# Optimization experiments

Hardware: AMD Instinct MI355X
Metric: run time of the kernel (lower is better)

## Reference

```python
import jax, jax.numpy as jnp
import numpy as np

N_NODES = 100000
N_EDGES = 6400000
F_IN = 128
F_OUT = 16


def setup_inputs() -> dict:
    key = jax.random.key(0)
    k1, k2, k3 = jax.random.split(key, 3)
    x = jax.random.normal(k1, (N_NODES, F_IN), dtype=jnp.float32)
    edge_index = jax.random.randint(k2, (2, N_EDGES), 0, N_NODES, dtype=jnp.int64)
    W = jax.random.normal(k3, (F_IN, F_OUT), dtype=jnp.float32) / np.sqrt(F_IN)
    b = jnp.zeros((F_OUT,), dtype=jnp.float32)
    return {"x": x, "edge_index": edge_index, "W": W, "b": b}


def reference(x, edge_index, W, b):
    # GCNConv (PyG defaults: add self-loops, symmetric normalization) -> tanh -> mean pool
    N = x.shape[0]
    loops = jnp.arange(N, dtype=edge_index.dtype)
    row = jnp.concatenate([edge_index[0], loops])  # source nodes
    col = jnp.concatenate([edge_index[1], loops])  # target nodes
    # degree of target nodes (edge weight 1.0)
    deg = jax.ops.segment_sum(jnp.ones(row.shape[0], dtype=x.dtype), col, num_segments=N)
    dinv = jnp.where(deg > 0, jax.lax.rsqrt(deg), 0.0)
    norm = dinv[row] * dinv[col]  # [E+N]
    h = x @ W  # [N, F_OUT] transform first (cheaper than transforming messages)
    msgs = h[row] * norm[:, None]  # gather + scale
    out = jax.ops.segment_sum(msgs, col, num_segments=N) + b  # scatter-add
    h = jnp.tanh(out)
    # MeanAggregation over all nodes -> single graph embedding [1, F_OUT]
    return jnp.mean(h, axis=0, keepdims=True)
```

## Files before the change

### kernel.cpp

```cpp
#include <hip/hip_runtime.h>
#include <math.h>

#define N_NODES 100000
#define N_EDGES 6400000
#define F_IN 128
#define F_OUT 16
#define NB 391
#define NBLK 1600
#define EPB 4000
#define LOCW 392
#define KPB 8
#define QSCALE 1024.0f
#define QINV   (1.0f / 1024.0f)
#define FIN_GRID 640

__global__ void __launch_bounds__(256) count_kernel(const int* __restrict__ col,
                                                    int* __restrict__ loc,
                                                    int* __restrict__ deg,
                                                    int* __restrict__ acc) {
    __shared__ int hist[NB];
    const int t = threadIdx.x, k = blockIdx.x;
    const int z0 = k * 63;
    for (int j = t; j < 63; j += 256)
        if (z0 + j < N_NODES) deg[z0 + j] = 0;
    const int a0 = k * 1000;
    for (int j = t; j < 1000; j += 256) acc[a0 + j] = 0;
    for (int i = t; i < NB; i += 256) hist[i] = 0;
    __syncthreads();
    const int e0 = k * EPB;
    for (int i = t; i < EPB; i += 256) atomicAdd(&hist[col[e0 + i] >> 8], 1);
    __syncthreads();
    for (int b = t; b < NB; b += 256) loc[k * LOCW + b] = hist[b];
}

__global__ void __launch_bounds__(256) desta_kernel(const int* __restrict__ loc,
        int* __restrict__ destT, int* __restrict__ total) {
    __shared__ int tsum[256];
    const int t = threadIdx.x, b = blockIdx.x;
    int v[7]; int s = 0;
    #pragma unroll
    for (int j = 0; j < 7; j++) {
        int k = t * 7 + j;
        v[j] = (k < NBLK) ? loc[k * LOCW + b] : 0;
        s += v[j];
    }
    tsum[t] = s;
    __syncthreads();
    for (int off = 1; off < 256; off <<= 1) {
        int a = (t >= off) ? tsum[t - off] : 0;
        __syncthreads();
        tsum[t] += a;
        __syncthreads();
    }
    int run = tsum[t] - s;
    #pragma unroll
    for (int j = 0; j < 7; j++) {
        int k = t * 7 + j;
        if (k < NBLK) destT[(size_t)b * NBLK + k] = run;
        run += v[j];
    }
    if (t == 255) total[b] = tsum[255];
}

__global__ void destb_kernel(const int* __restrict__ total, int* __restrict__ boffs) {
    __shared__ int lds[512];
    const int t = threadIdx.x;
    int v = (t < NB) ? total[t] : 0;
    lds[t] = v; __syncthreads();
    for (int off = 1; off < 512; off <<= 1) {
        int a = (t >= off) ? lds[t - off] : 0; __syncthreads();
        lds[t] += a; __syncthreads();
    }
    if (t < NB) boffs[t] = lds[t] - v;
    if (t == NB) boffs[NB] = N_EDGES;
}

__global__ void __launch_bounds__(256) place_kernel(const int* __restrict__ row,
        const int* __restrict__ col, const int* __restrict__ destT,
        const int* __restrict__ boffs, unsigned int* __restrict__ packed) {
    __shared__ int hist[NB];
    __shared__ int scanb[512];
    __shared__ int base[NB];
    __shared__ int gadj[NB];
    __shared__ unsigned int tile[EPB];
    __shared__ unsigned short tileb[EPB];
    const int t = threadIdx.x, k = blockIdx.x;
    const int e0 = k * EPB;
    int myc[16], myr[16];
    #pragma unroll
    for (int j = 0; j < 16; j++) {
        int idx = t + j * 256;
        if (idx < EPB) { myc[j] = col[e0 + idx]; myr[j] = row[e0 + idx]; }
        else { myc[j] = -1; myr[j] = 0; }
    }
    for (int i = t; i < NB; i += 256) hist[i] = 0;
    __syncthreads();
    #pragma unroll
    for (int j = 0; j < 16; j++)
        if (myc[j] >= 0) atomicAdd(&hist[myc[j] >> 8], 1);
    __syncthreads();
    scanb[t] = (t < NB) ? hist[t] : 0;
    scanb[t + 256] = (t + 256 < NB) ? hist[t + 256] : 0;
    __syncthreads();
    for (int off = 1; off < 512; off <<= 1) {
        int a  = (t >= off) ? scanb[t - off] : 0;
        int a2 = scanb[t + 256 - off];
        __syncthreads();
        scanb[t] += a; scanb[t + 256] += a2;
        __syncthreads();
    }
    if (t < NB) base[t] = scanb[t] - hist[t];
    if (t + 256 < NB) base[t + 256] = scanb[t + 256] - hist[t + 256];
    __syncthreads();
    for (int bb = t; bb < NB; bb += 256) {
        gadj[bb] = boffs[bb] + destT[(size_t)bb * NBLK + k] - base[bb];
        hist[bb] = 0;
    }
    __syncthreads();
    #pragma unroll
    for (int j = 0; j < 16; j++) {
        if (myc[j] >= 0) {
            int bb = myc[j] >> 8;
            int pos = base[bb] + atomicAdd(&hist[bb], 1);
            tile[pos] = ((unsigned)myr[j] << 8) | (unsigned)(myc[j] & 255);
            tileb[pos] = (unsigned short)bb;
        }
    }
    __syncthreads();
    for (int i = t; i < EPB; i += 256)
        packed[gadj[tileb[i]] + i] = tile[i];
}

__global__ void __launch_bounds__(256) deg_kernel(const unsigned int* __restrict__ packed,
        const int* __restrict__ boffs, int* __restrict__ deg) {
    __shared__ int dh[256];
    const int t = threadIdx.x;
    dh[t] = 0;
    __syncthreads();
    const int b = blockIdx.x, part = blockIdx.y;
    const int s = boffs[b], e = boffs[b + 1];
    const int chunk = (e - s + 3) >> 2;
    const int cs = s + part * chunk;
    const int ce = min(cs + chunk, e);
    for (int i = cs + t; i < ce; i += 256)
        atomicAdd(&dh[packed[i] & 255u], 1);
    __syncthreads();
    const int node = (b << 8) + t;
    if (node < N_NODES && dh[t]) atomicAdd(&deg[node], dh[t]);
}

__global__ void __launch_bounds__(256) gemm_kernel(const float* __restrict__ x,
        const float* __restrict__ W, const int* __restrict__ deg,
        short* __restrict__ gq) {
    __shared__ float Ws[F_IN * F_OUT];
    __shared__ float xs[16 * 132];
    const int tid = threadIdx.x;
    const int n0 = blockIdx.x * 16;
    const float4* W4 = (const float4*)W;
    for (int i = tid; i < 512; i += 256) ((float4*)Ws)[i] = W4[i];
    const float4* x4 = (const float4*)(x + (size_t)n0 * F_IN);
    for (int i = tid; i < 512; i += 256) {
        int n = i >> 5, j = i & 31;
        *(float4*)(xs + n * 132 + j * 4) = x4[i];
    }
    __syncthreads();
    const int node = tid >> 4, f = tid & 15;
    const float* xr = &xs[node * 132];
    float acc = 0.f;
    #pragma unroll 8
    for (int k = 0; k < F_IN; k++) acc += xr[k] * Ws[k * 16 + f];
    const float dinvn = rsqrtf((float)deg[n0 + node] + 1.0f);
    float v = acc * dinvn * QSCALE;
    v = fminf(fmaxf(v, -32000.f), 32000.f);
    gq[n0 * 16 + tid] = (short)__float2int_rn(v);
}

__global__ void __launch_bounds__(256) scatter_kernel(
        const unsigned int* __restrict__ packed, const int* __restrict__ boffs,
        const short* __restrict__ gq, int* __restrict__ acc) {
    __shared__ int sacc[256 * F_OUT];
    const int t = threadIdx.x;
    for (int i = t; i < 256 * F_OUT; i += 256) sacc[i] = 0;
    __syncthreads();
    const int b = blockIdx.x, part = blockIdx.y;
    const int s = boffs[b], e = boffs[b + 1];
    const int chunk = (e - s + KPB - 1) / KPB;
    const int cs = s + part * chunk;
    const int ce = min(cs + chunk, e);
    const int f = t & 15, eg = t >> 4;
    int i = cs + eg;
    for (; i + 112 < ce; i += 128) {
        unsigned p0 = packed[i];
        unsigned p1 = packed[i + 16];
        unsigned p2 = packed[i + 32];
        unsigned p3 = packed[i + 48];
        unsigned p4 = packed[i + 64];
        unsigned p5 = packed[i + 80];
        unsigned p6 = packed[i + 96];
        unsigned p7 = packed[i + 112];
        int v0 = gq[(p0 >> 8) * 16 + f];
        int v1 = gq[(p1 >> 8) * 16 + f];
        int v2 = gq[(p2 >> 8) * 16 + f];
        int v3 = gq[(p3 >> 8) * 16 + f];
        int v4 = gq[(p4 >> 8) * 16 + f];
        int v5 = gq[(p5 >> 8) * 16 + f];
        int v6 = gq[(p6 >> 8) * 16 + f];
        int v7 = gq[(p7 >> 8) * 16 + f];
        atomicAdd(&sacc[((p0 & 255u) << 4) + f], v0);
        atomicAdd(&sacc[((p1 & 255u) << 4) + f], v1);
        atomicAdd(&sacc[((p2 & 255u) << 4) + f], v2);
        atomicAdd(&sacc[((p3 & 255u) << 4) + f], v3);
        atomicAdd(&sacc[((p4 & 255u) << 4) + f], v4);
        atomicAdd(&sacc[((p5 & 255u) << 4) + f], v5);
        atomicAdd(&sacc[((p6 & 255u) << 4) + f], v6);
        atomicAdd(&sacc[((p7 & 255u) << 4) + f], v7);
    }
    for (; i < ce; i += 16) {
        unsigned p0 = packed[i];
        atomicAdd(&sacc[((p0 & 255u) << 4) + f], (int)gq[(p0 >> 8) * 16 + f]);
    }
    __syncthreads();
    const int nbase = b << 8;
    for (int j = t; j < 256 * F_OUT; j += 256) {
        int v = sacc[j];
        if (v && nbase + (j >> 4) < N_NODES)
            atomicAdd(&acc[((size_t)nbase << 4) + j], v);
    }
}

__global__ void __launch_bounds__(256) finalize_kernel(const int* __restrict__ acc,
        const short* __restrict__ gq, const int* __restrict__ deg,
        const float* __restrict__ b, double* __restrict__ dsum,
        int* __restrict__ done, float* __restrict__ out) {
    __shared__ float s[4][16];
    __shared__ int lastflag;
    const int tid = threadIdx.x;
    const int f = tid & 15;
    const float bf = b[f];
    float local = 0.f;
    for (int i = blockIdx.x * blockDim.x + tid; i < N_NODES * F_OUT;
         i += gridDim.x * blockDim.x) {
        const int n = i >> 4;
        int ai = acc[i] + (int)gq[i];
        float dinvn = rsqrtf((float)deg[n] + 1.0f);
        local += tanhf(dinvn * ((float)ai * QINV) + bf);
    }
    local += __shfl_down(local, 32);
    local += __shfl_down(local, 16);
    const int lane = tid & 63, wave = tid >> 6;
    if (lane < 16) s[wave][lane] = local;
    __syncthreads();
    if (tid < 16) {
        float v = s[0][tid] + s[1][tid] + s[2][tid] + s[3][tid];
        atomicAdd(&dsum[tid], (double)v);
    }
    if (tid == 0) {
        __threadfence();
        lastflag = (atomicAdd(done, 1) == (int)gridDim.x - 1);
    }
    __syncthreads();
    if (lastflag && tid < 16) {
        double v = atomicAdd(&dsum[tid], 0.0);
        out[tid] = (float)(v * (1.0 / (double)N_NODES));
    }
}

extern "C" void kernel_launch(void* const* d_in, const int* in_sizes, int n_in,
                              void* d_out, int out_size, void* d_ws, size_t ws_size,
                              hipStream_t stream) {
    const float* x  = (const float*)d_in[0];
    const int*   ei = (const int*)d_in[1];
    const float* W  = (const float*)d_in[2];
    const float* b  = (const float*)d_in[3];
    float* out = (float*)d_out;

    const int* row = ei;
    const int* col = ei + N_EDGES;

    char* p = (char*)d_ws;
    double*       dsum   = (double*)p;        p += 16 * 8;
    int*          done   = (int*)p;           p += 16;
    int*          total  = (int*)p;           p += 1568;
    int*          boffs  = (int*)p;           p += (NB + 1) * 4;
    int*          deg    = (int*)p;           p += (size_t)N_NODES * 4;
    short*        gq     = (short*)p;         p += (size_t)N_NODES * F_OUT * 2;
    unsigned int* packed = (unsigned int*)p;  p += (size_t)N_EDGES * 4;
    int*          acc    = (int*)p;           p += (size_t)N_NODES * F_OUT * 4;
    int*          loc    = (int*)p;           p += (size_t)NBLK * LOCW * 4;
    int*          destT  = (int*)p;

    hipMemsetAsync(dsum, 0, 16 * 8 + 16, stream);

    count_kernel   <<<NBLK, 256, 0, stream>>>(col, loc, deg, acc);
    desta_kernel   <<<NB, 256, 0, stream>>>(loc, destT, total);
    destb_kernel   <<<1, 512, 0, stream>>>(total, boffs);
    place_kernel   <<<NBLK, 256, 0, stream>>>(row, col, destT, boffs, packed);
    deg_kernel     <<<dim3(NB, 4), 256, 0, stream>>>(packed, boffs, deg);
    gemm_kernel    <<<N_NODES / 16, 256, 0, stream>>>(x, W, deg, gq);
    scatter_kernel <<<dim3(NB, KPB), 256, 0, stream>>>(packed, boffs, gq, acc);
    finalize_kernel<<<FIN_GRID, 256, 0, stream>>>(acc, gq, deg, b, dsum, done, out);
}
```

Baseline: 267.7 us.

## Replace exact bucket prefix-scan with fixed-capacity buckets and atomic cursors

Drops the count, two-level scan and separate degree kernels. Edges are now placed into fixed-capacity per-bucket regions (BCAP slots each) using atomic cursors, and degrees are computed with global atomics inside the placement kernel. The GEMM is retiled to 128 nodes per block with 4x2 register blocking, and it also zeroes the accumulator. Scatter splits each bucket into 5 parts with a shallower unroll. This cuts kernel launches and extra passes over the edge list, but adds contended global atomics and relies on no bucket exceeding the fixed capacity.

Measured after the change: 500.9 us. 87.1% more time.

```diff
diff --git a/kernel.cpp b/kernel.cpp
--- a/kernel.cpp
+++ b/kernel.cpp
@@ -8,76 +8,17 @@
 #define NB 391
 #define NBLK 1600
 #define EPB 4000
-#define LOCW 392
-#define KPB 8
+#define BCAP 20480
+#define KPB 5
 #define QSCALE 1024.0f
 #define QINV   (1.0f / 1024.0f)
 #define FIN_GRID 640
-
-__global__ void __launch_bounds__(256) count_kernel(const int* __restrict__ col,
-                                                    int* __restrict__ loc,
-                                                    int* __restrict__ deg,
-                                                    int* __restrict__ acc) {
-    __shared__ int hist[NB];
-    const int t = threadIdx.x, k = blockIdx.x;
-    const int z0 = k * 63;
-    for (int j = t; j < 63; j += 256)
-        if (z0 + j < N_NODES) deg[z0 + j] = 0;
-    const int a0 = k * 1000;
-    for (int j = t; j < 1000; j += 256) acc[a0 + j] = 0;
-    for (int i = t; i < NB; i += 256) hist[i] = 0;
-    __syncthreads();
-    const int e0 = k * EPB;
-    for (int i = t; i < EPB; i += 256) atomicAdd(&hist[col[e0 + i] >> 8], 1);
-    __syncthreads();
-    for (int b = t; b < NB; b += 256) loc[k * LOCW + b] = hist[b];
-}
-
-__global__ void __launch_bounds__(256) desta_kernel(const int* __restrict__ loc,
-        int* __restrict__ destT, int* __restrict__ total) {
-    __shared__ int tsum[256];
-    const int t = threadIdx.x, b = blockIdx.x;
-    int v[7]; int s = 0;
-    #pragma unroll
-    for (int j = 0; j < 7; j++) {
-        int k = t * 7 + j;
-        v[j] = (k < NBLK) ? loc[k * LOCW + b] : 0;
-        s += v[j];
-    }
-    tsum[t] = s;
-    __syncthreads();
-    for (int off = 1; off < 256; off <<= 1) {
-        int a = (t >= off) ? tsum[t - off] : 0;
-        __syncthreads();
-        tsum[t] += a;
-        __syncthreads();
-    }
-    int run = tsum[t] - s;
-    #pragma unroll
-    for (int j = 0; j < 7; j++) {
-        int k = t * 7 + j;
-        if (k < NBLK) destT[(size_t)b * NBLK + k] = run;
-        run += v[j];
-    }
-    if (t == 255) total[b] = tsum[255];
-}
-
-__global__ void destb_kernel(const int* __restrict__ total, int* __restrict__ boffs) {
-    __shared__ int lds[512];
-    const int t = threadIdx.x;
-    int v = (t < NB) ? total[t] : 0;
-    lds[t] = v; __syncthreads();
-    for (int off = 1; off < 512; off <<= 1) {
-        int a = (t >= off) ? lds[t - off] : 0; __syncthreads();
-        lds[t] += a; __syncthreads();
-    }
-    if (t < NB) boffs[t] = lds[t] - v;
-    if (t == NB) boffs[NB] = N_EDGES;
-}
+#define GN 128
+#define GSTRIDE 132
 
 __global__ void __launch_bounds__(256) place_kernel(const int* __restrict__ row,
-        const int* __restrict__ col, const int* __restrict__ destT,
-        const int* __restrict__ boffs, unsigned int* __restrict__ packed) {
+        const int* __restrict__ col, int* __restrict__ cur,
+        int* __restrict__ deg, unsigned int* __restrict__ packed) {
     __shared__ int hist[NB];
     __shared__ int scanb[512];
     __shared__ int base[NB];
@@ -96,8 +37,12 @@
     for (int i = t; i < NB; i += 256) hist[i] = 0;
     __syncthreads();
     #pragma unroll
-    for (int j = 0; j < 16; j++)
-        if (myc[j] >= 0) atomicAdd(&hist[myc[j] >> 8], 1);
+    for (int j = 0; j < 16; j++) {
+        if (myc[j] >= 0) {
+            atomicAdd(&hist[myc[j] >> 8], 1);
+            atomicAdd(&deg[myc[j]], 1);
+        }
+    }
     __syncthreads();
     scanb[t] = (t < NB) ? hist[t] : 0;
     scanb[t + 256] = (t + 256 < NB) ? hist[t + 256] : 0;
@@ -113,7 +58,9 @@
     if (t + 256 < NB) base[t + 256] = scanb[t + 256] - hist[t + 256];
     __syncthreads();
     for (int bb = t; bb < NB; bb += 256) {
-        gadj[bb] = boffs[bb] + destT[(size_t)bb * NBLK + k] - base[bb];
+        int c = hist[bb];
+        int g = (c > 0) ? atomicAdd(&cur[bb], c) : 0;
+        gadj[bb] = bb * BCAP + g - base[bb];
         hist[bb] = 0;
     }
     __syncthreads();
@@ -131,89 +78,103 @@
         packed[gadj[tileb[i]] + i] = tile[i];
 }
 
-__global__ void __launch_bounds__(256) deg_kernel(const unsigned int* __restrict__ packed,
-        const int* __restrict__ boffs, int* __restrict__ deg) {
-    __shared__ int dh[256];
-    const int t = threadIdx.x;
-    dh[t] = 0;
-    __syncthreads();
-    const int b = blockIdx.x, part = blockIdx.y;
-    const int s = boffs[b], e = boffs[b + 1];
-    const int chunk = (e - s + 3) >> 2;
-    const int cs = s + part * chunk;
-    const int ce = min(cs + chunk, e);
-    for (int i = cs + t; i < ce; i += 256)
-        atomicAdd(&dh[packed[i] & 255u], 1);
-    __syncthreads();
-    const int node = (b << 8) + t;
-    if (node < N_NODES && dh[t]) atomicAdd(&deg[node], dh[t]);
-}
-
 __global__ void __launch_bounds__(256) gemm_kernel(const float* __restrict__ x,
         const float* __restrict__ W, const int* __restrict__ deg,
-        short* __restrict__ gq) {
+        short* __restrict__ gq, int* __restrict__ acc) {
     __shared__ float Ws[F_IN * F_OUT];
-    __shared__ float xs[16 * 132];
-    const int tid = threadIdx.x;
-    const int n0 = blockIdx.x * 16;
+    __shared__ float xs[GN * GSTRIDE];
+    const int t = threadIdx.x;
+    const int n0 = blockIdx.x * GN;
+    {
+        const size_t z0 = (size_t)blockIdx.x * 2048;
+        for (int j = t; j < 2048; j += 256) {
+            size_t idx = z0 + j;
+            if (idx < (size_t)N_NODES * F_OUT) acc[idx] = 0;
+        }
+    }
     const float4* W4 = (const float4*)W;
-    for (int i = tid; i < 512; i += 256) ((float4*)Ws)[i] = W4[i];
-    const float4* x4 = (const float4*)(x + (size_t)n0 * F_IN);
-    for (int i = tid; i < 512; i += 256) {
-        int n = i >> 5, j = i & 31;
-        *(float4*)(xs + n * 132 + j * 4) = x4[i];
-    }
-    __syncthreads();
-    const int node = tid >> 4, f = tid & 15;
-    const float* xr = &xs[node * 132];
-    float acc = 0.f;
+    for (int i = t; i < 512; i += 256) ((float4*)Ws)[i] = W4[i];
+    for (int i = t; i < GN * 32; i += 256) {
+        int r = i >> 5, c4 = i & 31;
+        float4 v = make_float4(0.f, 0.f, 0.f, 0.f);
+        if (n0 + r < N_NODES)
+            v = ((const float4*)(x + (size_t)(n0 + r) * F_IN))[c4];
+        *(float4*)(xs + r * GSTRIDE + c4 * 4) = v;
+    }
+    __syncthreads();
+    const int fq = t & 3, n2 = t >> 2;
+    const float* xrA = xs + n2 * GSTRIDE;
+    const float* xrB = xs + (n2 + 64) * GSTRIDE;
+    float accA[4] = {0.f, 0.f, 0.f, 0.f};
+    float accB[4] = {0.f, 0.f, 0.f, 0.f};
     #pragma unroll 8
-    for (int k = 0; k < F_IN; k++) acc += xr[k] * Ws[k * 16 + f];
-    const float dinvn = rsqrtf((float)deg[n0 + node] + 1.0f);
-    float v = acc * dinvn * QSCALE;
-    v = fminf(fmaxf(v, -32000.f), 32000.f);
-    gq[n0 * 16 + tid] = (short)__float2int_rn(v);
+    for (int kq = 0; kq < 32; kq++) {
+        float4 xa = *(const float4*)(xrA + kq * 4);
+        float4 xb = *(const float4*)(xrB + kq * 4);
+        #pragma unroll
+        for (int j = 0; j < 4; j++) {
+            float4 w = *(const float4*)(Ws + (kq * 4 + j) * 16 + fq * 4);
+            float a = (j == 0) ? xa.x : (j == 1) ? xa.y : (j == 2) ? xa.z : xa.w;
+            float bv = (j == 0) ? xb.x : (j == 1) ? xb.y : (j == 2) ? xb.z : xb.w;
+            accA[0] += a * w.x;  accA[1] += a * w.y;
+            accA[2] += a * w.z;  accA[3] += a * w.w;
+            accB[0] += bv * w.x; accB[1] += bv * w.y;
+            accB[2] += bv * w.z; accB[3] += bv * w.w;
+        }
+    }
+    const int gA = n0 + n2, gB = n0 + n2 + 64;
+    if (gA < N_NODES) {
+        float dinv = rsqrtf((float)deg[gA] + 1.0f);
+        short4 o;
+        float v0 = fminf(fmaxf(accA[0] * dinv * QSCALE, -32000.f), 32000.f);
+        float v1 = fminf(fmaxf(accA[1] * dinv * QSCALE, -32000.f), 32000.f);
+        float v2 = fminf(fmaxf(accA[2] * dinv * QSCALE, -32000.f), 32000.f);
+        float v3 = fminf(fmaxf(accA[3] * dinv * QSCALE, -32000.f), 32000.f);
+        o.x = (short)__float2int_rn(v0); o.y = (short)__float2int_rn(v1);
+        o.z = (short)__float2int_rn(v2); o.w = (short)__float2int_rn(v3);
+        *(short4*)(gq + (size_t)gA * 16 + fq * 4) = o;
+    }
+    if (gB < N_NODES) {
+        float dinv = rsqrtf((float)deg[gB] + 1.0f);
+        short4 o;
+        float v0 = fminf(fmaxf(accB[0] * dinv * QSCALE, -32000.f), 32000.f);
+        float v1 = fminf(fmaxf(accB[1] * dinv * QSCALE, -32000.f), 32000.f);
+        float v2 = fminf(fmaxf(accB[2] * dinv * QSCALE, -32000.f), 32000.f);
+        float v3 = fminf(fmaxf(accB[3] * dinv * QSCALE, -32000.f), 32000.f);
+        o.x = (short)__float2int_rn(v0); o.y = (short)__float2int_rn(v1);
+        o.z = (short)__float2int_rn(v2); o.w = (short)__float2int_rn(v3);
+        *(short4*)(gq + (size_t)gB * 16 + fq * 4) = o;
+    }
 }
 
 __global__ void __launch_bounds__(256) scatter_kernel(
-        const unsigned int* __restrict__ packed, const int* __restrict__ boffs,
+        const unsigned int* __restrict__ packed, const int* __restrict__ cur,
         const short* __restrict__ gq, int* __restrict__ acc) {
     __shared__ int sacc[256 * F_OUT];
     const int t = threadIdx.x;
     for (int i = t; i < 256 * F_OUT; i += 256) sacc[i] = 0;
     __syncthreads();
     const int b = blockIdx.x, part = blockIdx.y;
-    const int s = boffs[b], e = boffs[b + 1];
-    const int chunk = (e - s + KPB - 1) / KPB;
+    const int cnt = cur[b];
+    const int s = b * BCAP;
+    const int chunk = (cnt + KPB - 1) / KPB;
     const int cs = s + part * chunk;
-    const int ce = min(cs + chunk, e);
+    const int ce = s + min((part + 1) * chunk, cnt);
     const int f = t & 15, eg = t >> 4;
     int i = cs + eg;
-    for (; i + 112 < ce; i += 128) {
+    for (; i + 48 < ce; i += 64) {
         unsigned p0 = packed[i];
         unsigned p1 = packed[i + 16];
         unsigned p2 = packed[i + 32];
         unsigned p3 = packed[i + 48];
-        unsigned p4 = packed[i + 64];
-        unsigned p5 = packed[i + 80];
-        unsigned p6 = packed[i + 96];
-        unsigned p7 = packed[i + 112];
         int v0 = gq[(p0 >> 8) * 16 + f];
         int v1 = gq[(p1 >> 8) * 16 + f];
         int v2 = gq[(p2 >> 8) * 16 + f];
         int v3 = gq[(p3 >> 8) * 16 + f];
-        int v4 = gq[(p4 >> 8) * 16 + f];
-        int v5 = gq[(p5 >> 8) * 16 + f];
-        int v6 = gq[(p6 >> 8) * 16 + f];
-        int v7 = gq[(p7 >> 8) * 16 + f];
         atomicAdd(&sacc[((p0 & 255u) << 4) + f], v0);
         atomicAdd(&sacc[((p1 & 255u) << 4) + f], v1);
         atomicAdd(&sacc[((p2 & 255u) << 4) + f], v2);
         atomicAdd(&sacc[((p3 & 255u) << 4) + f], v3);
-        atomicAdd(&sacc[((p4 & 255u) << 4) + f], v4);
-        atomicAdd(&sacc[((p5 & 255u) << 4) + f], v5);
-        atomicAdd(&sacc[((p6 & 255u) << 4) + f], v6);
-        atomicAdd(&sacc[((p7 & 255u) << 4) + f], v7);
     }
     for (; i < ce; i += 16) {
         unsigned p0 = packed[i];
@@ -278,25 +239,18 @@
     const int* col = ei + N_EDGES;
 
     char* p = (char*)d_ws;
-    double*       dsum   = (double*)p;        p += 16 * 8;
-    int*          done   = (int*)p;           p += 16;
-    int*          total  = (int*)p;           p += 1568;
-    int*          boffs  = (int*)p;           p += (NB + 1) * 4;
+    double*       dsum   = (double*)p;        p += 128;
+    int*          done   = (int*)p;           p += 32;
+    int*          cur    = (int*)p;           p += 1600;
     int*          deg    = (int*)p;           p += (size_t)N_NODES * 4;
+    int*          acc    = (int*)p;           p += (size_t)N_NODES * F_OUT * 4;
     short*        gq     = (short*)p;         p += (size_t)N_NODES * F_OUT * 2;
-    unsigned int* packed = (unsigned int*)p;  p += (size_t)N_EDGES * 4;
-    int*          acc    = (int*)p;           p += (size_t)N_NODES * F_OUT * 4;
-    int*          loc    = (int*)p;           p += (size_t)NBLK * LOCW * 4;
-    int*          destT  = (int*)p;
-
-    hipMemsetAsync(dsum, 0, 16 * 8 + 16, stream);
-
-    count_kernel   <<<NBLK, 256, 0, stream>>>(col, loc, deg, acc);
-    desta_kernel   <<<NB, 256, 0, stream>>>(loc, destT, total);
-    destb_kernel   <<<1, 512, 0, stream>>>(total, boffs);
-    place_kernel   <<<NBLK, 256, 0, stream>>>(row, col, destT, boffs, packed);
-    deg_kernel     <<<dim3(NB, 4), 256, 0, stream>>>(packed, boffs, deg);
-    gemm_kernel    <<<N_NODES / 16, 256, 0, stream>>>(x, W, deg, gq);
-    scatter_kernel <<<dim3(NB, KPB), 256, 0, stream>>>(packed, boffs, gq, acc);
+    unsigned int* packed = (unsigned int*)p;
+
+    hipMemsetAsync(dsum, 0, 128 + 32 + 1600 + (size_t)N_NODES * 4, stream);
+
+    place_kernel   <<<NBLK, 256, 0, stream>>>(row, col, cur, deg, packed);
+    gemm_kernel    <<<(N_NODES + GN - 1) / GN, 256, 0, stream>>>(x, W, deg, gq, acc);
+    scatter_kernel <<<dim3(NB, KPB), 256, 0, stream>>>(packed, cur, gq, acc);
     finalize_kernel<<<FIN_GRID, 256, 0, stream>>>(acc, gq, deg, b, dsum, done, out);
 }
```
